# Kernel optimization log

Hardware: AMD Instinct MI355X
Metric: run time of the kernel (lower is better)

Reference implementation:

```python
import jax, jax.numpy as jnp
import numpy as np

N = 100_000      # nodes
E = 1_200_000    # edges per graph (avg degree 12)
D = 64           # args.hidden
PROP_STEP = 8
LAM = 1.0
ALP = 1.0 / (LAM + 1.0)   # args.alp <= 0 -> 1/(lam+1)
LAM0 = 1.0
K = 4
LAM_K = 0.5


def setup_inputs() -> dict:
    key = jax.random.key(0)
    k0, k1, k2, k3, k4 = jax.random.split(key, 5)
    x = jax.random.normal(k0, (N, D), dtype=jnp.float32)
    src0 = jax.random.randint(k1, (E,), 0, N, dtype=jnp.int32)
    # ensure every node has in-degree >= 1 (no isolated dst nodes)
    dst0 = jnp.concatenate([jnp.arange(N, dtype=jnp.int32),
                            jax.random.randint(k2, (E - N,), 0, N, dtype=jnp.int32)])
    src1 = jax.random.randint(k3, (E,), 0, N, dtype=jnp.int32)
    dst1 = jnp.concatenate([jnp.arange(N, dtype=jnp.int32),
                            jax.random.randint(k4, (E - N,), 0, N, dtype=jnp.int32)])
    return {"x": x, "src0": src0, "dst0": dst0, "src1": src1, "dst1": dst1}


def _in_degrees(dst):
    # DGL in_degrees(): count of incoming edges per node
    return jax.ops.segment_sum(jnp.ones(dst.shape, jnp.float32), dst, num_segments=N)


def _normalized_AX(src, dst, inv_sqrt_deg, Y):
    # Y <- D^{-1/2} A D^{-1/2} Y  (edge weight w = 1)
    Yn = Y * inv_sqrt_deg                                    # [N, D]
    agg = jax.ops.segment_sum(Yn[src], dst, num_segments=N)  # gather/scatter SpMM
    return agg * inv_sqrt_deg


def reference(x, src0, dst0, src1, dst1):
    deg0 = _in_degrees(dst0)
    deg1 = _in_degrees(dst1)
    # D^{-1/2} with inf -> 0 (as in D_power_X)
    inv0 = jnp.where(deg0 > 0, deg0 ** -0.5, 0.0)[:, None]
    inv1 = jnp.where(deg1 > 0, deg1 ** -0.5, 0.0)[:, None]
    D0 = deg0[:, None]
    D1 = deg1[:, None]
    Y = x
    for _ in range(PROP_STEP):
        nAX0 = _normalized_AX(src0, dst0, inv0, Y)
        nAX1 = _normalized_AX(src1, dst1, inv1, Y)
        Y = Y - ALP * (LAM0 * (Y - x) / (D0 + D1)
                       + LAM * (Y - nAX0)
                       - (LAM_K / K) * (Y - nAX1))
    return Y
```

## Files before the change

kernel.cpp:

```cpp
#include <hip/hip_runtime.h>
#include <hip/hip_fp16.h>

#define NN 100000
#define NE 1200000
#define DIM 64
#define NBINS 391
#define NBE 128
#define CHUNK (NE / NBE)
#define NBLK ((NN + 255) / 256)
#define NPH 7


__global__ void __launch_bounds__(256) bin_count(const int* __restrict__ dst0,
                                                 const int* __restrict__ dst1,
                                                 int* __restrict__ blk_cnt) {
    __shared__ int c[NBINS];
    int t = threadIdx.x;
    for (int i = t; i < NBINS; i += 256) c[i] = 0;
    __syncthreads();
    int lo = blockIdx.x * CHUNK, hi = lo + CHUNK;
    for (int e = lo + t; e < hi; e += 256) {
        atomicAdd(&c[dst0[e] >> 8], 1);
        atomicAdd(&c[dst1[e] >> 8], 1);
    }
    __syncthreads();
    for (int i = t; i < NBINS; i += 256) blk_cnt[blockIdx.x * NBINS + i] = c[i];
}

__global__ void __launch_bounds__(512) bin_scan(const int* __restrict__ blk_cnt,
                                                int* __restrict__ bin_start) {
    __shared__ int tot[512];
    int t = threadIdx.x;
    int s = 0;
    if (t < NBINS)
        for (int b = 0; b < NBE; ++b) s += blk_cnt[b * NBINS + t];
    tot[t] = s;
    __syncthreads();
    for (int off = 1; off < 512; off <<= 1) {
        int v = (t >= off) ? tot[t - off] : 0;
        __syncthreads();
        tot[t] += v;
        __syncthreads();
    }
    if (t <= NBINS) bin_start[t] = tot[t] - s;
}

__global__ void __launch_bounds__(NBE) blk_base_k(const int* __restrict__ blk_cnt,
                                                  const int* __restrict__ bin_start,
                                                  int* __restrict__ blk_base) {
    __shared__ int s[NBE];
    int b = blockIdx.x, t = threadIdx.x;
    int v = blk_cnt[t * NBINS + b];
    s[t] = v;
    __syncthreads();
    for (int off = 1; off < NBE; off <<= 1) {
        int x = (t >= off) ? s[t - off] : 0;
        __syncthreads();
        s[t] += x;
        __syncthreads();
    }
    blk_base[t * NBINS + b] = bin_start[b] + s[t] - v;
}

__global__ void __launch_bounds__(256) bin_permute(const int* __restrict__ src0,
                                                   const int* __restrict__ dst0,
                                                   const int* __restrict__ src1,
                                                   const int* __restrict__ dst1,
                                                   const int* __restrict__ blk_base,
                                                   int2* __restrict__ binned) {
    __shared__ int off[NBINS];
    int t = threadIdx.x;
    for (int i = t; i < NBINS; i += 256) off[i] = blk_base[blockIdx.x * NBINS + i];
    __syncthreads();
    int lo = blockIdx.x * CHUNK, hi = lo + CHUNK;
    for (int e = lo + t; e < hi; e += 256) {
        int s = src0[e], d = dst0[e];
        int p = atomicAdd(&off[d >> 8], 1);
        binned[p] = make_int2(s, d);
        s = src1[e]; d = dst1[e];
        p = atomicAdd(&off[d >> 8], 1);
        binned[p] = make_int2(s, d | (1 << 20));
    }
}

__global__ void __launch_bounds__(256) deg_count(const int2* __restrict__ binned,
                                                 const int* __restrict__ bin_start,
                                                 int* __restrict__ deg0,
                                                 int* __restrict__ deg1) {
    __shared__ int dg[512];
    int b = blockIdx.x, t = threadIdx.x;
    dg[t] = 0; dg[t + 256] = 0;
    __syncthreads();
    int lo = bin_start[b], hi = bin_start[b + 1];
    for (int i = lo + t; i < hi; i += 256) {
        int2 r = binned[i];
        int d = r.y & 0xFFFFF, g = r.y >> 20;
        atomicAdd(&dg[((d & 255) << 1) | g], 1);
    }
    __syncthreads();
    int n = b * 256 + t;
    if (n < NN) { deg0[n] = dg[t << 1]; deg1[n] = dg[(t << 1) | 1]; }
}

__global__ void __launch_bounds__(256) scan_l1(const int* __restrict__ deg0,
                                               const int* __restrict__ deg1,
                                               int* __restrict__ rs, int* __restrict__ dp,
                                               int* __restrict__ bs) {
    __shared__ int s0[256];
    int t = threadIdx.x;
    int n = blockIdx.x * 256 + t;
    int a = 0;
    if (n < NN) a = (deg0[n] + deg1[n] + 7) & ~7;
    s0[t] = a;
    __syncthreads();
    for (int off = 1; off < 256; off <<= 1) {
        int x0 = (t >= off) ? s0[t - off] : 0;
        __syncthreads();
        s0[t] += x0;
        __syncthreads();
    }
    if (n < NN) { rs[n] = s0[t] - a; dp[n] = a; }
    if (t == 255) bs[blockIdx.x] = s0[255];
}

__global__ void __launch_bounds__(512) scan_l2(int* __restrict__ bs) {
    __shared__ int s0[512];
    int t = threadIdx.x;
    int a = (t < NBLK) ? bs[t] : 0;
    s0[t] = a;
    __syncthreads();
    for (int off = 1; off < 512; off <<= 1) {
        int x0 = (t >= off) ? s0[t - off] : 0;
        __syncthreads();
        s0[t] += x0;
        __syncthreads();
    }
    if (t < NBLK) bs[t] = s0[t] - a;
}

__global__ void __launch_bounds__(256) scan_l3(int* __restrict__ rs, const int* __restrict__ bs) {
    int n = blockIdx.x * 256 + threadIdx.x;
    if (n < NN) rs[n] += bs[blockIdx.x];
}

__global__ void node_params(const int* __restrict__ deg0, const int* __restrict__ deg1,
                            float2* __restrict__ nsc, float* __restrict__ sc,
                            float* __restrict__ cy) {
    int n = blockIdx.x * blockDim.x + threadIdx.x;
    if (n < NN) {
        int a = deg0[n], b = deg1[n];
        nsc[n] = make_float2((a > 0) ? 0.5f * rsqrtf((float)a) : 0.0f,
                             (b > 0) ? -0.0625f * rsqrtf((float)b) : 0.0f);
        int s = a + b;
        float rD = (s > 0) ? 1.0f / (float)s : 0.0f;
        sc[n] = 0.5625f - 0.5f * rD;
        cy[n] = 0.5f * rD;
    }
}

__global__ void pad_fill(const int* __restrict__ deg0, const int* __restrict__ deg1,
                         const int* __restrict__ dp, const int* __restrict__ rs,
                         int* __restrict__ es) {
    int n = blockIdx.x * blockDim.x + threadIdx.x;
    if (n < NN) {
        int b = rs[n] + deg0[n] + deg1[n], e = rs[n] + dp[n];
        for (int i = b; i < e; ++i) es[i] = 0;
    }
}

__global__ void __launch_bounds__(256) csr_scatter(const int2* __restrict__ binned,
                                                   const int* __restrict__ bin_start,
                                                   const int* __restrict__ rs,
                                                   const int* __restrict__ deg0,
                                                   const int* __restrict__ deg1,
                                                   int* __restrict__ es) {
    __shared__ int cur[256];
    int b = blockIdx.x, t = threadIdx.x;
    cur[t] = 0;
    __syncthreads();
    int lo = bin_start[b], hi = bin_start[b + 1];
    for (int ph = 0; ph < NPH; ++ph) {
        for (int i = lo + t; i < hi; i += 256) {
            int2 r = binned[i];
            int sN = r.x;
            if ((sN >> 14) != ph) continue;
            int d = r.y & 0xFFFFF, g = r.y >> 20;
            int dg = g ? deg1[sN] : deg0[sN];
            int p = atomicAdd(&cur[d & 255], 1);
            es[rs[d] + p] = sN | (g << 17) | (dg << 18);
        }
        __syncthreads();
    }
}

__global__ void convert_x(const float* __restrict__ X, const float* __restrict__ cy,
                          __half* __restrict__ HA, __half* __restrict__ BX) {
    int i = blockIdx.x * blockDim.x + threadIdx.x;
    if (i < NN * DIM / 4) {
        float4 v = ((const float4*)X)[i];
        float c = cy[i >> 4];
        ushort4 a, b;
        a.x = __half_as_ushort(__float2half(v.x));
        a.y = __half_as_ushort(__float2half(v.y));
        a.z = __half_as_ushort(__float2half(v.z));
        a.w = __half_as_ushort(__float2half(v.w));
        b.x = __half_as_ushort(__float2half(v.x * c));
        b.y = __half_as_ushort(__float2half(v.y * c));
        b.z = __half_as_ushort(__float2half(v.z * c));
        b.w = __half_as_ushort(__float2half(v.w * c));
        ((ushort4*)HA)[i] = a;
        ((ushort4*)BX)[i] = b;
    }
}

__global__ void __launch_bounds__(256) step_kernel(
    const __half* __restrict__ Yh, const __half* __restrict__ BX,
    const int* __restrict__ rs, const int* __restrict__ dp,
    const int* __restrict__ es, const float2* __restrict__ nsc,
    const float* __restrict__ sc,
    __half* __restrict__ Yho, float* __restrict__ Ffo)
{
    __shared__ float lut[128];
    for (int i = threadIdx.x; i < 128; i += 256)
        lut[i] = (i == 0) ? 0.0f : rsqrtf((float)i);
    __syncthreads();

    int node = blockIdx.x * 4 + (threadIdx.x >> 6);
    int d = threadIdx.x & 63;
    int un = __builtin_amdgcn_readfirstlane(node);
    int s  = __builtin_amdgcn_readfirstlane(rs[un]);
    int c  = __builtin_amdgcn_readfirstlane(dp[un]);
    float2 ns = nsc[un];

    float acc = 0.0f;
    int eb[8];
#pragma unroll
    for (int k = 0; k < 8; ++k) eb[k] = es[s + k];
    for (int i = 0; i < c; i += 8) {
        int en[8];
#pragma unroll
        for (int k = 0; k < 8; ++k) en[k] = es[s + i + 8 + k];
        float yv[8];
#pragma unroll
        for (int k = 0; k < 8; ++k)
            yv[k] = __half2float(Yh[(size_t)(eb[k] & 0x1FFFF) * DIM + d]);
#pragma unroll
        for (int k = 0; k < 8; ++k) {
            float wsc = (eb[k] & (1 << 17)) ? ns.y : ns.x;
            acc = fmaf(yv[k], wsc * lut[eb[k] >> 18], acc);
        }
#pragma unroll
        for (int k = 0; k < 8; ++k) eb[k] = en[k];
    }
    float y  = __half2float(Yh[(size_t)un * DIM + d]);
    float bx = __half2float(BX[(size_t)un * DIM + d]);
    float o = fmaf(sc[un], y, bx) + acc;
    if (Ffo) Ffo[(size_t)un * DIM + d] = o;
    else     Yho[(size_t)un * DIM + d] = __float2half(o);
}

extern "C" void kernel_launch(void* const* d_in, const int* in_sizes, int n_in,
                              void* d_out, int out_size, void* d_ws, size_t ws_size,
                              hipStream_t stream) {
    const float* x   = (const float*)d_in[0];
    const int* src0  = (const int*)d_in[1];
    const int* dst0  = (const int*)d_in[2];
    const int* src1  = (const int*)d_in[3];
    const int* dst1  = (const int*)d_in[4];
    float* out = (float*)d_out;

    char* ws = (char*)d_ws;
    size_t off = 0;
    auto alloc = [&](size_t bytes) -> void* {
        void* p = ws + off;
        off += (bytes + 255) & ~(size_t)255;
        return p;
    };

    const size_t ES_CAP = (size_t)2 * NE + 8 * NN + 64;

    __half* HA   = (__half*)alloc((size_t)NN * DIM * 2);
    __half* HB   = (__half*)alloc((size_t)NN * DIM * 2);
    __half* BX   = (__half*)alloc((size_t)NN * DIM * 2);
    int2*   binned = (int2*)alloc((size_t)2 * NE * 8);
    int*    es   = (int*)alloc(ES_CAP * 4);
    int*    blk_cnt  = (int*)alloc((size_t)NBE * NBINS * 4);
    int*    blk_base = (int*)alloc((size_t)NBE * NBINS * 4);
    int*    bin_st   = (int*)alloc((size_t)(NBINS + 1) * 4);
    int*    deg0 = (int*)alloc((size_t)NN * 4);
    int*    deg1 = (int*)alloc((size_t)NN * 4);
    int*    rs   = (int*)alloc((size_t)NN * 4);
    int*    dp   = (int*)alloc((size_t)NN * 4);
    float2* nsc  = (float2*)alloc((size_t)NN * 8);
    float*  sc   = (float*)alloc((size_t)NN * 4);
    float*  cy   = (float*)alloc((size_t)NN * 4);
    int*    bs   = (int*)alloc((size_t)NBLK * 4);

    const int TB = 256;
    bin_count<<<NBE, 256, 0, stream>>>(dst0, dst1, blk_cnt);
    bin_scan<<<1, 512, 0, stream>>>(blk_cnt, bin_st);
    blk_base_k<<<NBINS, NBE, 0, stream>>>(blk_cnt, bin_st, blk_base);
    bin_permute<<<NBE, 256, 0, stream>>>(src0, dst0, src1, dst1, blk_base, binned);
    deg_count<<<NBINS, 256, 0, stream>>>(binned, bin_st, deg0, deg1);
    scan_l1<<<NBLK, 256, 0, stream>>>(deg0, deg1, rs, dp, bs);
    scan_l2<<<1, 512, 0, stream>>>(bs);
    scan_l3<<<NBLK, 256, 0, stream>>>(rs, bs);
    node_params<<<(NN + TB - 1) / TB, TB, 0, stream>>>(deg0, deg1, nsc, sc, cy);
    pad_fill<<<(NN + TB - 1) / TB, TB, 0, stream>>>(deg0, deg1, dp, rs, es);
    csr_scatter<<<NBINS, 256, 0, stream>>>(binned, bin_st, rs, deg0, deg1, es);
    convert_x<<<(NN * DIM / 4 + TB - 1) / TB, TB, 0, stream>>>(x, cy, HA, BX);

    int grid = NN / 4;
    for (int i = 0; i < 8; ++i) {
        const __half* hin = (i & 1) ? HB : HA;
        __half* hout = (i & 1) ? HA : HB;
        float* fout = (i == 7) ? out : nullptr;
        step_kernel<<<grid, TB, 0, stream>>>(hin, BX, rs, dp, es, nsc, sc, hout, fout);
    }
}
```

Before: 608.6 us.

## Pack binned edges into 32-bit words and build CSR with a single counting-sort pass

Binned edge records shrink from an int2 (src, dst) to one 32-bit word holding the source id, the graph bit and the low 8 bits of the destination, which halves that buffer's traffic. csr_scatter first builds a per-phase, per-destination histogram in shared memory and turns it into exclusive offsets. It then places every edge in one pass instead of re-reading the bin seven times, keeping the phase ordering by source. The separate pad_fill kernel is folded into csr_scatter's tail, which removes one launch. The cost is a larger shared-memory histogram and two reads of the bin.

```diff
diff --git a/kernel.cpp b/kernel.cpp
--- a/kernel.cpp
+++ b/kernel.cpp
@@ -67,7 +67,7 @@
                                                    const int* __restrict__ src1,
                                                    const int* __restrict__ dst1,
                                                    const int* __restrict__ blk_base,
-                                                   int2* __restrict__ binned) {
+                                                   unsigned int* __restrict__ binned) {
     __shared__ int off[NBINS];
     int t = threadIdx.x;
     for (int i = t; i < NBINS; i += 256) off[i] = blk_base[blockIdx.x * NBINS + i];
@@ -76,14 +76,14 @@
     for (int e = lo + t; e < hi; e += 256) {
         int s = src0[e], d = dst0[e];
         int p = atomicAdd(&off[d >> 8], 1);
-        binned[p] = make_int2(s, d);
+        binned[p] = (unsigned)s | ((unsigned)(d & 255) << 18);
         s = src1[e]; d = dst1[e];
         p = atomicAdd(&off[d >> 8], 1);
-        binned[p] = make_int2(s, d | (1 << 20));
-    }
-}
-
-__global__ void __launch_bounds__(256) deg_count(const int2* __restrict__ binned,
+        binned[p] = (unsigned)s | (1u << 17) | ((unsigned)(d & 255) << 18);
+    }
+}
+
+__global__ void __launch_bounds__(256) deg_count(const unsigned int* __restrict__ binned,
                                                  const int* __restrict__ bin_start,
                                                  int* __restrict__ deg0,
                                                  int* __restrict__ deg1) {
@@ -93,9 +93,9 @@
     __syncthreads();
     int lo = bin_start[b], hi = bin_start[b + 1];
     for (int i = lo + t; i < hi; i += 256) {
-        int2 r = binned[i];
-        int d = r.y & 0xFFFFF, g = r.y >> 20;
-        atomicAdd(&dg[((d & 255) << 1) | g], 1);
+        unsigned r = binned[i];
+        int dlow = (r >> 18) & 255, g = (r >> 17) & 1;
+        atomicAdd(&dg[(dlow << 1) | g], 1);
     }
     __syncthreads();
     int n = b * 256 + t;
@@ -158,38 +158,49 @@
     }
 }
 
-__global__ void pad_fill(const int* __restrict__ deg0, const int* __restrict__ deg1,
-                         const int* __restrict__ dp, const int* __restrict__ rs,
-                         int* __restrict__ es) {
-    int n = blockIdx.x * blockDim.x + threadIdx.x;
-    if (n < NN) {
-        int b = rs[n] + deg0[n] + deg1[n], e = rs[n] + dp[n];
-        for (int i = b; i < e; ++i) es[i] = 0;
-    }
-}
-
-__global__ void __launch_bounds__(256) csr_scatter(const int2* __restrict__ binned,
+__global__ void __launch_bounds__(256) csr_scatter(const unsigned int* __restrict__ binned,
                                                    const int* __restrict__ bin_start,
                                                    const int* __restrict__ rs,
                                                    const int* __restrict__ deg0,
                                                    const int* __restrict__ deg1,
                                                    int* __restrict__ es) {
-    __shared__ int cur[256];
+    __shared__ int hist[8 * 256];
+    __shared__ int rsl[256];
+    __shared__ int degsum[256];
     int b = blockIdx.x, t = threadIdx.x;
-    cur[t] = 0;
+    int n = b * 256 + t;
+    rsl[t] = (n < NN) ? rs[n] : 0;
+    for (int i = t; i < 8 * 256; i += 256) hist[i] = 0;
     __syncthreads();
     int lo = bin_start[b], hi = bin_start[b + 1];
-    for (int ph = 0; ph < NPH; ++ph) {
-        for (int i = lo + t; i < hi; i += 256) {
-            int2 r = binned[i];
-            int sN = r.x;
-            if ((sN >> 14) != ph) continue;
-            int d = r.y & 0xFFFFF, g = r.y >> 20;
-            int dg = g ? deg1[sN] : deg0[sN];
-            int p = atomicAdd(&cur[d & 255], 1);
-            es[rs[d] + p] = sN | (g << 17) | (dg << 18);
+    for (int i = lo + t; i < hi; i += 256) {
+        unsigned r = binned[i];
+        int ph = (r & 0x1FFFF) >> 14;
+        atomicAdd(&hist[ph * 256 + ((r >> 18) & 255)], 1);
+    }
+    __syncthreads();
+    {
+        int acc = 0;
+        for (int ph = 0; ph < NPH; ++ph) {
+            int v = hist[ph * 256 + t];
+            hist[ph * 256 + t] = acc;
+            acc += v;
         }
-        __syncthreads();
+        degsum[t] = acc;
+    }
+    __syncthreads();
+    for (int i = lo + t; i < hi; i += 256) {
+        unsigned r = binned[i];
+        int sN = r & 0x1FFFF, g = (r >> 17) & 1, dlow = (r >> 18) & 255;
+        int ph = sN >> 14;
+        int p = atomicAdd(&hist[ph * 256 + dlow], 1);
+        int dgv = g ? deg1[sN] : deg0[sN];
+        es[rsl[dlow] + p] = sN | (g << 17) | (dgv << 18);
+    }
+    __syncthreads();
+    if (n < NN) {
+        int base = rsl[t], ds = degsum[t], dpv = (ds + 7) & ~7;
+        for (int i = base + ds; i < base + dpv; ++i) es[i] = 0;
     }
 }
 
@@ -282,7 +293,7 @@
     __half* HA   = (__half*)alloc((size_t)NN * DIM * 2);
     __half* HB   = (__half*)alloc((size_t)NN * DIM * 2);
     __half* BX   = (__half*)alloc((size_t)NN * DIM * 2);
-    int2*   binned = (int2*)alloc((size_t)2 * NE * 8);
+    unsigned int* binned = (unsigned int*)alloc((size_t)2 * NE * 4);
     int*    es   = (int*)alloc(ES_CAP * 4);
     int*    blk_cnt  = (int*)alloc((size_t)NBE * NBINS * 4);
     int*    blk_base = (int*)alloc((size_t)NBE * NBINS * 4);
@@ -306,7 +317,6 @@
     scan_l2<<<1, 512, 0, stream>>>(bs);
     scan_l3<<<NBLK, 256, 0, stream>>>(rs, bs);
     node_params<<<(NN + TB - 1) / TB, TB, 0, stream>>>(deg0, deg1, nsc, sc, cy);
-    pad_fill<<<(NN + TB - 1) / TB, TB, 0, stream>>>(deg0, deg1, dp, rs, es);
     csr_scatter<<<NBINS, 256, 0, stream>>>(binned, bin_st, rs, deg0, deg1, es);
     convert_x<<<(NN * DIM / 4 + TB - 1) / TB, TB, 0, stream>>>(x, cy, HA, BX);
 
```

New measurement: 534.7 us. -12.1%, faster.
